# Optimization experiments

Measured on AMD Instinct MI355X. Metric: run time of the kernel, lower is better.

## Reference

```python
import jax, jax.numpy as jnp
import numpy as np

LATENT_DIM = 256
CODEBOOK_SIZE = 8192
COMMITMENT_WEIGHT = 0.25
CODEBOOK_WEIGHT = 1.0


def setup_inputs() -> dict:
    key = jax.random.key(0)
    k1, k2 = jax.random.split(key)
    latents = jax.random.normal(k1, (16, 1024, LATENT_DIM), dtype=jnp.float32)
    patch_mask = jnp.ones((16, 1024), dtype=jnp.float32)
    # nn.init.uniform_(codebook.weight, -1/K, 1/K)
    codebook = jax.random.uniform(
        k2, (CODEBOOK_SIZE, LATENT_DIM), dtype=jnp.float32,
        minval=-1.0 / CODEBOOK_SIZE, maxval=1.0 / CODEBOOK_SIZE)
    return {"latents": latents, "patch_mask": patch_mask, "codebook": codebook}


def reference(latents, patch_mask, codebook):
    B, P, D = latents.shape
    flat = latents.reshape(-1, D)  # [N, D]
    # squared euclidean distances [N, K]
    distances = (
        jnp.sum(flat * flat, axis=1, keepdims=True)
        + jnp.sum(codebook * codebook, axis=1)
        - 2.0 * flat @ codebook.T
    )
    symbol_ids = jnp.argmin(distances, axis=1)          # [N]
    quantized = codebook[symbol_ids].reshape(B, P, D)   # [B, P, D]
    symbol_ids = symbol_ids.reshape(B, P)

    st_quantized = latents + jax.lax.stop_gradient(quantized - latents)
    commitment_loss = jnp.mean((latents - jax.lax.stop_gradient(quantized)) ** 2) * COMMITMENT_WEIGHT
    codebook_loss = jnp.mean((quantized - jax.lax.stop_gradient(latents)) ** 2) * CODEBOOK_WEIGHT

    # perplexity: masked codeword usage histogram without materializing one-hot
    denom = jnp.maximum(jnp.sum(patch_mask), 1.0)
    avg_probs = jax.ops.segment_sum(
        patch_mask.reshape(-1), symbol_ids.reshape(-1),
        num_segments=CODEBOOK_SIZE) / denom
    perplexity = jnp.exp(-jnp.sum(avg_probs * jnp.log(avg_probs + 1e-8)))

    return symbol_ids, quantized, st_quantized, commitment_loss, codebook_loss, perplexity
```

## Files before the change

kernel.cpp:

```cpp
#include <hip/hip_runtime.h>
#include <math.h>

#define DD 256
#define KK 8192
#define NN 16384
#define MT 16
#define RPW 8
#define NT 512
#define NCHG 8
#define NBM (NN / MT)
#define NBLOCKS 512
#define RSTRIDE 260

#define OUT_IDS   0
#define OUT_Q     16384
#define OUT_ST    4210688
#define OUT_COMMIT 8404992
#define OUT_CBL    8404993
#define OUT_PERP   8404994

__device__ __forceinline__ float np_block128_sumsq(const float* p) {
    #pragma clang fp contract(off)
    float r0 = p[0] * p[0], r1 = p[1] * p[1], r2 = p[2] * p[2], r3 = p[3] * p[3];
    float r4 = p[4] * p[4], r5 = p[5] * p[5], r6 = p[6] * p[6], r7 = p[7] * p[7];
    for (int i = 8; i < 128; i += 8) {
        r0 = r0 + p[i + 0] * p[i + 0];
        r1 = r1 + p[i + 1] * p[i + 1];
        r2 = r2 + p[i + 2] * p[i + 2];
        r3 = r3 + p[i + 3] * p[i + 3];
        r4 = r4 + p[i + 4] * p[i + 4];
        r5 = r5 + p[i + 5] * p[i + 5];
        r6 = r6 + p[i + 6] * p[i + 6];
        r7 = r7 + p[i + 7] * p[i + 7];
    }
    return ((r0 + r1) + (r2 + r3)) + ((r4 + r5) + (r6 + r7));
}

__device__ __forceinline__ float np_pairwise256_sumsq(const float* a) {
    #pragma clang fp contract(off)
    float s0 = np_block128_sumsq(a);
    float s1 = np_block128_sumsq(a + 128);
    return s0 + s1;
}

__global__ __launch_bounds__(256) void rowsumsq(const float* __restrict__ A,
                                                float* __restrict__ out) {
    __shared__ __align__(16) float sA[64][RSTRIDE];
    const int tid = threadIdx.x;
    const int base = blockIdx.x * 64;
    #pragma unroll
    for (int i = 0; i < 16; ++i) {
        int g = i * 256 + tid;
        int row = g >> 6, d4 = g & 63;
        float4 v = reinterpret_cast<const float4*>(A)[(size_t)(base + row) * (DD / 4) + d4];
        *reinterpret_cast<float4*>(&sA[row][d4 * 4]) = v;
    }
    __syncthreads();
    if (tid < 64) out[base + tid] = np_pairwise256_sumsq(sA[tid]);
}

__global__ __launch_bounds__(256) void cb_transpose(const float* __restrict__ CB,
                                                    float4* __restrict__ CBt) {
    const int id = blockIdx.x * 256 + threadIdx.x;
    const int p   = id >> 13;
    const int col = id & (KK - 1);
    CBt[id] = *reinterpret_cast<const float4*>(CB + (size_t)col * DD + p * 4);
}

__global__ __launch_bounds__(256) void vq_main(const float* __restrict__ X,
                                               const float4* __restrict__ CBt,
                                               const float* __restrict__ c2,
                                               const float* __restrict__ x2,
                                               const float* __restrict__ mask,
                                               float* __restrict__ out,
                                               float* __restrict__ hist) {
    __shared__ float gbest[2][MT];
    __shared__ int   gidx[2][MT];

    const int tid  = threadIdx.x;
    const int lane = tid & 63;
    const int wid  = tid >> 6;
    const int widu = __builtin_amdgcn_readfirstlane(wid);
    const int g    = wid >> 1;
    const int gu   = widu >> 1;
    const int wg   = wid & 1;
    const int wgu  = widu & 1;
    const int block_row = blockIdx.x * MT;

    const float* xr = X + (size_t)(block_row + wgu * RPW) * DD;

    float x2r[RPW];
    #pragma unroll
    for (int rr = 0; rr < RPW; ++rr) x2r[rr] = x2[block_row + wg * RPW + rr];

    float best[RPW];
    int   besti[RPW];
    #pragma unroll
    for (int rr = 0; rr < RPW; ++rr) { best[rr] = 3.4e38f; besti[rr] = 0; }

    const float4* cbt_lane = CBt + lane;

    for (int ch = 0; ch < NCHG; ++ch) {
        const int chg = gu * NCHG + ch;
        float c2v[8];
        #pragma unroll
        for (int j = 0; j < 8; ++j) c2v[j] = c2[chg * NT + lane + 64 * j];

        float acc[8][8];
        #pragma unroll
        for (int rr = 0; rr < 8; ++rr)
            #pragma unroll
            for (int j = 0; j < 8; ++j) acc[rr][j] = 0.0f;

        const float4* cbase = cbt_lane + (size_t)chg * NT;

        for (int b = 0; b < 8; ++b) {
            #pragma unroll
            for (int t = 0; t < 8; ++t) {
                const int p = b * 8 + t;
                const float4* src = cbase + (size_t)p * KK;
                #pragma unroll
                for (int jh = 0; jh < 2; ++jh) {
                    float4 cc[4];
                    #pragma unroll
                    for (int j = 0; j < 4; ++j) cc[j] = src[64 * (jh * 4 + j)];
                    #pragma unroll
                    for (int rr = 0; rr < 8; ++rr) {
                        const float sx = xr[rr * DD + p * 4 + 0];
                        const float sy = xr[rr * DD + p * 4 + 1];
                        const float sz = xr[rr * DD + p * 4 + 2];
                        const float sw = xr[rr * DD + p * 4 + 3];
                        #pragma unroll
                        for (int j = 0; j < 4; ++j) {
                            float& a = acc[rr][jh * 4 + j];
                            a = fmaf(sx, cc[j].x, a);
                            a = fmaf(sy, cc[j].y, a);
                            a = fmaf(sz, cc[j].z, a);
                            a = fmaf(sw, cc[j].w, a);
                        }
                    }
                }
            }
        }

        #pragma unroll
        for (int rr = 0; rr < 8; ++rr) {
            #pragma unroll
            for (int j = 0; j < 8; ++j) {
                const int col = chg * NT + lane + 64 * j;
                float t1 = x2r[rr] + c2v[j];
                float sc = t1 - 2.0f * acc[rr][j];
                if (sc < best[rr] || (sc == best[rr] && col < besti[rr])) {
                    best[rr] = sc; besti[rr] = col;
                }
            }
        }
    }

    #pragma unroll
    for (int rr = 0; rr < RPW; ++rr) {
        float b = best[rr];
        int  bi = besti[rr];
        #pragma unroll
        for (int m = 32; m > 0; m >>= 1) {
            float b2 = __shfl_xor(b, m, 64);
            int   i2 = __shfl_xor(bi, m, 64);
            if (b2 < b || (b2 == b && i2 < bi)) { b = b2; bi = i2; }
        }
        if (lane == 0) {
            gbest[g][wg * RPW + rr] = b;
            gidx [g][wg * RPW + rr] = bi;
        }
    }
    __syncthreads();

    if (tid < MT) {
        const float b0 = gbest[0][tid], b1 = gbest[1][tid];
        const int bi = (b1 < b0) ? gidx[1][tid] : gidx[0][tid];
        out[OUT_IDS + block_row + tid] = (float)bi;
        atomicAdd(&hist[bi], mask[block_row + tid]);
    }
}

__global__ __launch_bounds__(256) void vq_gather(const float* __restrict__ X,
                                                 const float* __restrict__ CB,
                                                 float* __restrict__ out,
                                                 float* __restrict__ partial) {
    __shared__ int   row_id[32];
    __shared__ float wsum[4];
    const int tid  = threadIdx.x;
    const int lane = tid & 63;
    const int wid  = tid >> 6;
    const int block_row = blockIdx.x * 32;

    if (tid < 32) row_id[tid] = (int)out[OUT_IDS + block_row + tid];
    __syncthreads();

    float msep = 0.0f;
    float* outq  = out + OUT_Q;
    float* outst = out + OUT_ST;
    #pragma unroll
    for (int i = 0; i < 8; ++i) {
        int g2 = i * 256 + tid;
        int row = g2 >> 6;
        int d4  = g2 & 63;
        int id  = row_id[row];
        float4 q = reinterpret_cast<const float4*>(CB)[(size_t)id * (DD / 4) + d4];
        float4 x = reinterpret_cast<const float4*>(X)[(size_t)(block_row + row) * (DD / 4) + d4];
        float4 st;
        st.x = x.x + (q.x - x.x);
        st.y = x.y + (q.y - x.y);
        st.z = x.z + (q.z - x.z);
        st.w = x.w + (q.w - x.w);
        float dx = x.x - q.x; msep = fmaf(dx, dx, msep);
        dx = x.y - q.y; msep = fmaf(dx, dx, msep);
        dx = x.z - q.z; msep = fmaf(dx, dx, msep);
        dx = x.w - q.w; msep = fmaf(dx, dx, msep);
        size_t o = (size_t)(block_row + row) * (DD / 4) + d4;
        reinterpret_cast<float4*>(outq)[o]  = q;
        reinterpret_cast<float4*>(outst)[o] = st;
    }
    #pragma unroll
    for (int off = 32; off > 0; off >>= 1) msep += __shfl_down(msep, off, 64);
    if (lane == 0) wsum[wid] = msep;
    __syncthreads();
    if (tid == 0) partial[blockIdx.x] = wsum[0] + wsum[1] + wsum[2] + wsum[3];
}

__global__ __launch_bounds__(256) void vq_finalize(const float* __restrict__ partial,
                                                   const float* __restrict__ hist,
                                                   float* __restrict__ out) {
    __shared__ double red[256];
    const int tid = threadIdx.x;

    double ps = 0.0;
    for (int j = tid; j < NBLOCKS; j += 256) ps += (double)partial[j];
    red[tid] = ps;
    __syncthreads();
    for (int s = 128; s > 0; s >>= 1) {
        if (tid < s) red[tid] += red[tid + s];
        __syncthreads();
    }
    double mse_sum = red[0];
    __syncthreads();

    double hs = 0.0;
    for (int j = tid; j < KK; j += 256) hs += (double)hist[j];
    red[tid] = hs;
    __syncthreads();
    for (int s = 128; s > 0; s >>= 1) {
        if (tid < s) red[tid] += red[tid + s];
        __syncthreads();
    }
    double denom = red[0] > 1.0 ? red[0] : 1.0;
    __syncthreads();

    double ent = 0.0;
    for (int j = tid; j < KK; j += 256) {
        double p = (double)hist[j] / denom;
        ent += p * log(p + 1e-8);
    }
    red[tid] = ent;
    __syncthreads();
    for (int s = 128; s > 0; s >>= 1) {
        if (tid < s) red[tid] += red[tid + s];
        __syncthreads();
    }

    if (tid == 0) {
        double mse = mse_sum / (double)((size_t)NN * DD);
        out[OUT_COMMIT] = (float)(mse * 0.25);
        out[OUT_CBL]    = (float)mse;
        out[OUT_PERP]   = (float)exp(-red[0]);
    }
}

extern "C" void kernel_launch(void* const* d_in, const int* in_sizes, int n_in,
                              void* d_out, int out_size, void* d_ws, size_t ws_size,
                              hipStream_t stream) {
    const float* latents = (const float*)d_in[0];
    const float* mask    = (const float*)d_in[1];
    const float* cb      = (const float*)d_in[2];
    float* out = (float*)d_out;

    float* hist    = (float*)d_ws;
    float* partial = hist + KK;
    float* c2      = partial + NBLOCKS;
    float* x2      = c2 + KK;

    float4* cbt = reinterpret_cast<float4*>(out + OUT_Q);

    hipMemsetAsync(d_ws, 0, KK * sizeof(float), stream);
    rowsumsq<<<KK / 64, 256, 0, stream>>>(cb, c2);
    rowsumsq<<<NN / 64, 256, 0, stream>>>(latents, x2);
    cb_transpose<<<(64 * KK) / 256, 256, 0, stream>>>(cb, cbt);
    vq_main<<<NBM, 256, 0, stream>>>(latents, cbt, c2, x2, mask, out, hist);
    vq_gather<<<NBLOCKS, 256, 0, stream>>>(latents, cb, out, partial);
    vq_finalize<<<1, 256, 0, stream>>>(partial, hist, out);
}
```

Before: 934.1 us.

## Transpose latents and double-buffer codebook loads in distance GEMM

Adds a kernel that transposes the latents into float4-interleaved layout (stored in the st_quantized output region as scratch), so each step's 8-row x values sit contiguously. The inner loop is rewritten with two register buffers of eight float4 codebook values, prefetching the next slice while FMAs run on the current one. The aim is to hide global load latency and make the uniform x loads cheaper. The cost is an extra transpose pass over the latents and higher register pressure from sixteen float4 buffers plus the 64 accumulators.

```diff
diff --git a/kernel.cpp b/kernel.cpp
--- a/kernel.cpp
+++ b/kernel.cpp
@@ -67,7 +67,37 @@
     CBt[id] = *reinterpret_cast<const float4*>(CB + (size_t)col * DD + p * 4);
 }
 
-__global__ __launch_bounds__(256) void vq_main(const float* __restrict__ X,
+__global__ __launch_bounds__(256) void x_transpose(const float* __restrict__ X,
+                                                   float4* __restrict__ Xt) {
+    const int id = blockIdx.x * 256 + threadIdx.x;
+    const int p   = id >> 14;
+    const int row = id & (NN - 1);
+    Xt[id] = *reinterpret_cast<const float4*>(X + (size_t)row * DD + p * 4);
+}
+
+#define LOADCC(dst, ptr) do {                                                  \
+    _Pragma("unroll")                                                          \
+    for (int j_ = 0; j_ < 8; ++j_) (dst)[j_] = (ptr)[64 * j_];                 \
+} while (0)
+
+#define FMASTEP(cc, xs) do {                                                   \
+    _Pragma("unroll")                                                          \
+    for (int rr_ = 0; rr_ < 8; ++rr_) {                                        \
+        const float sx_ = (xs)[rr_ * 4 + 0];                                   \
+        const float sy_ = (xs)[rr_ * 4 + 1];                                   \
+        const float sz_ = (xs)[rr_ * 4 + 2];                                   \
+        const float sw_ = (xs)[rr_ * 4 + 3];                                   \
+        _Pragma("unroll")                                                      \
+        for (int j_ = 0; j_ < 8; ++j_) {                                       \
+            acc[rr_][j_] = fmaf(sx_, (cc)[j_].x, acc[rr_][j_]);                \
+            acc[rr_][j_] = fmaf(sy_, (cc)[j_].y, acc[rr_][j_]);                \
+            acc[rr_][j_] = fmaf(sz_, (cc)[j_].z, acc[rr_][j_]);                \
+            acc[rr_][j_] = fmaf(sw_, (cc)[j_].w, acc[rr_][j_]);                \
+        }                                                                      \
+    }                                                                          \
+} while (0)
+
+__global__ __launch_bounds__(256) void vq_main(const float4* __restrict__ Xt,
                                                const float4* __restrict__ CBt,
                                                const float* __restrict__ c2,
                                                const float* __restrict__ x2,
@@ -87,7 +117,8 @@
     const int wgu  = widu & 1;
     const int block_row = blockIdx.x * MT;
 
-    const float* xr = X + (size_t)(block_row + wgu * RPW) * DD;
+    const float* xbase = reinterpret_cast<const float*>(Xt)
+                       + (size_t)(block_row + wgu * RPW) * 4;
 
     float x2r[RPW];
     #pragma unroll
@@ -112,36 +143,24 @@
             #pragma unroll
             for (int j = 0; j < 8; ++j) acc[rr][j] = 0.0f;
 
-        const float4* cbase = cbt_lane + (size_t)chg * NT;
-
-        for (int b = 0; b < 8; ++b) {
-            #pragma unroll
-            for (int t = 0; t < 8; ++t) {
-                const int p = b * 8 + t;
-                const float4* src = cbase + (size_t)p * KK;
-                #pragma unroll
-                for (int jh = 0; jh < 2; ++jh) {
-                    float4 cc[4];
-                    #pragma unroll
-                    for (int j = 0; j < 4; ++j) cc[j] = src[64 * (jh * 4 + j)];
-                    #pragma unroll
-                    for (int rr = 0; rr < 8; ++rr) {
-                        const float sx = xr[rr * DD + p * 4 + 0];
-                        const float sy = xr[rr * DD + p * 4 + 1];
-                        const float sz = xr[rr * DD + p * 4 + 2];
-                        const float sw = xr[rr * DD + p * 4 + 3];
-                        #pragma unroll
-                        for (int j = 0; j < 4; ++j) {
-                            float& a = acc[rr][jh * 4 + j];
-                            a = fmaf(sx, cc[j].x, a);
-                            a = fmaf(sy, cc[j].y, a);
-                            a = fmaf(sz, cc[j].z, a);
-                            a = fmaf(sw, cc[j].w, a);
-                        }
-                    }
-                }
-            }
+        float4 ccA[8], ccB[8];
+        const float4* pA = cbt_lane + (size_t)chg * NT;
+        const float4* pB = pA + KK;
+        const float*  xs = xbase;
+
+        LOADCC(ccA, pA);
+        for (int pb = 0; pb < 31; ++pb) {
+            LOADCC(ccB, pB);
+            FMASTEP(ccA, xs);
+            pA += 2 * KK;
+            LOADCC(ccA, pA);
+            FMASTEP(ccB, xs + NN * 4);
+            pB += 2 * KK;
+            xs += 2 * NN * 4;
         }
+        LOADCC(ccB, pB);
+        FMASTEP(ccA, xs);
+        FMASTEP(ccB, xs + NN * 4);
 
         #pragma unroll
         for (int rr = 0; rr < 8; ++rr) {
@@ -289,12 +308,14 @@
     float* x2      = c2 + KK;
 
     float4* cbt = reinterpret_cast<float4*>(out + OUT_Q);
+    float4* xt  = reinterpret_cast<float4*>(out + OUT_ST);
 
     hipMemsetAsync(d_ws, 0, KK * sizeof(float), stream);
     rowsumsq<<<KK / 64, 256, 0, stream>>>(cb, c2);
     rowsumsq<<<NN / 64, 256, 0, stream>>>(latents, x2);
     cb_transpose<<<(64 * KK) / 256, 256, 0, stream>>>(cb, cbt);
-    vq_main<<<NBM, 256, 0, stream>>>(latents, cbt, c2, x2, mask, out, hist);
+    x_transpose<<<(64 * NN) / 256, 256, 0, stream>>>(latents, xt);
+    vq_main<<<NBM, 256, 0, stream>>>(xt, cbt, c2, x2, mask, out, hist);
     vq_gather<<<NBLOCKS, 256, 0, stream>>>(latents, cb, out, partial);
     vq_finalize<<<1, 256, 0, stream>>>(partial, hist, out);
 }
```

Measured after the change: 975.9 us. +4.5%, slower.

## Stream codebook tiles into LDS with async global_load_lds double buffering

Applied to the files above, without the earlier changes.

Changes the transposed codebook layout so that each chunk group's 64 d-slices sit contiguously. The main distance loop now prefetches each slice into a per-wave double-buffered LDS region using global_load_lds, with explicit vmcnt/lgkmcnt waits, before reading it back from LDS for the FMAs. This is meant to hide global memory latency behind compute and to stream loads sequentially. In exchange it adds 64KB of LDS per block, which can lower occupancy, and relies on hand-placed waitcnt and sched_barrier calls for correctness.

```diff
diff --git a/kernel.cpp b/kernel.cpp
--- a/kernel.cpp
+++ b/kernel.cpp
@@ -11,6 +11,7 @@
 #define NBM (NN / MT)
 #define NBLOCKS 512
 #define RSTRIDE 260
+#define NPL 512
 
 #define OUT_IDS   0
 #define OUT_Q     16384
@@ -18,6 +19,12 @@
 #define OUT_COMMIT 8404992
 #define OUT_CBL    8404993
 #define OUT_PERP   8404994
+
+__device__ __forceinline__ void gl2lds16(const float* g, float* l) {
+    __builtin_amdgcn_global_load_lds(
+        (const __attribute__((address_space(1))) float*)g,
+        (__attribute__((address_space(3))) float*)l, 16, 0, 0);
+}
 
 __device__ __forceinline__ float np_block128_sumsq(const float* p) {
     #pragma clang fp contract(off)
@@ -59,21 +66,25 @@
     if (tid < 64) out[base + tid] = np_pairwise256_sumsq(sA[tid]);
 }
 
-__global__ __launch_bounds__(256) void cb_transpose(const float* __restrict__ CB,
-                                                    float4* __restrict__ CBt) {
+__global__ __launch_bounds__(256) void cb_transpose2(const float* __restrict__ CB,
+                                                     float4* __restrict__ CBt2) {
     const int id = blockIdx.x * 256 + threadIdx.x;
-    const int p   = id >> 13;
-    const int col = id & (KK - 1);
-    CBt[id] = *reinterpret_cast<const float4*>(CB + (size_t)col * DD + p * 4);
+    const int q  = id >> 9;
+    const int cw = id & 511;
+    const int chg = q >> 6;
+    const int p   = q & 63;
+    const int col = chg * 512 + cw;
+    CBt2[id] = *reinterpret_cast<const float4*>(CB + (size_t)col * DD + p * 4);
 }
 
 __global__ __launch_bounds__(256) void vq_main(const float* __restrict__ X,
-                                               const float4* __restrict__ CBt,
+                                               const float4* __restrict__ CBt2,
                                                const float* __restrict__ c2,
                                                const float* __restrict__ x2,
                                                const float* __restrict__ mask,
                                                float* __restrict__ out,
                                                float* __restrict__ hist) {
+    __shared__ __align__(16) float sCC[4 * 4096];
     __shared__ float gbest[2][MT];
     __shared__ int   gidx[2][MT];
 
@@ -87,6 +98,11 @@
     const int wgu  = widu & 1;
     const int block_row = blockIdx.x * MT;
 
+    float* const dl0 = &sCC[widu * 4096];
+    float* const dl1 = dl0 + 2048;
+    const float* const sl0 = dl0 + lane * 4;
+    const float* const sl1 = sl0 + 2048;
+
     const float* xr = X + (size_t)(block_row + wgu * RPW) * DD;
 
     float x2r[RPW];
@@ -98,7 +114,14 @@
     #pragma unroll
     for (int rr = 0; rr < RPW; ++rr) { best[rr] = 3.4e38f; besti[rr] = 0; }
 
-    const float4* cbt_lane = CBt + lane;
+    const float4* srcq = CBt2 + (size_t)gu * NPL * 512 + lane;
+
+    #pragma unroll
+    for (int k = 0; k < 8; ++k) gl2lds16((const float*)(srcq + k * 64), dl0 + k * 256);
+    srcq += 512;
+    #pragma unroll
+    for (int k = 0; k < 8; ++k) gl2lds16((const float*)(srcq + k * 64), dl1 + k * 256);
+    srcq += 512;
 
     for (int ch = 0; ch < NCHG; ++ch) {
         const int chg = gu * NCHG + ch;
@@ -112,33 +135,42 @@
             #pragma unroll
             for (int j = 0; j < 8; ++j) acc[rr][j] = 0.0f;
 
-        const float4* cbase = cbt_lane + (size_t)chg * NT;
-
-        for (int b = 0; b < 8; ++b) {
+        #pragma unroll 2
+        for (int p = 0; p < 64; ++p) {
+            const int q = ch * 64 + p;
+
+            if (q == NPL - 1) { asm volatile("s_waitcnt vmcnt(0)" ::: "memory"); }
+            else              { asm volatile("s_waitcnt vmcnt(8)" ::: "memory"); }
+            __builtin_amdgcn_sched_barrier(0);
+
+            const float* sb = (q & 1) ? sl1 : sl0;
+            float4 cc[8];
             #pragma unroll
-            for (int t = 0; t < 8; ++t) {
-                const int p = b * 8 + t;
-                const float4* src = cbase + (size_t)p * KK;
+            for (int j = 0; j < 8; ++j)
+                cc[j] = *reinterpret_cast<const float4*>(sb + j * 256);
+            asm volatile("s_waitcnt lgkmcnt(0)" ::: "memory");
+            __builtin_amdgcn_sched_barrier(0);
+
+            if (q < NPL - 2) {
+                float* db = (q & 1) ? dl1 : dl0;
                 #pragma unroll
-                for (int jh = 0; jh < 2; ++jh) {
-                    float4 cc[4];
-                    #pragma unroll
-                    for (int j = 0; j < 4; ++j) cc[j] = src[64 * (jh * 4 + j)];
-                    #pragma unroll
-                    for (int rr = 0; rr < 8; ++rr) {
-                        const float sx = xr[rr * DD + p * 4 + 0];
-                        const float sy = xr[rr * DD + p * 4 + 1];
-                        const float sz = xr[rr * DD + p * 4 + 2];
-                        const float sw = xr[rr * DD + p * 4 + 3];
-                        #pragma unroll
-                        for (int j = 0; j < 4; ++j) {
-                            float& a = acc[rr][jh * 4 + j];
-                            a = fmaf(sx, cc[j].x, a);
-                            a = fmaf(sy, cc[j].y, a);
-                            a = fmaf(sz, cc[j].z, a);
-                            a = fmaf(sw, cc[j].w, a);
-                        }
-                    }
+                for (int k = 0; k < 8; ++k)
+                    gl2lds16((const float*)(srcq + k * 64), db + k * 256);
+                srcq += 512;
+            }
+
+            #pragma unroll
+            for (int rr = 0; rr < 8; ++rr) {
+                const float sx = xr[rr * DD + p * 4 + 0];
+                const float sy = xr[rr * DD + p * 4 + 1];
+                const float sz = xr[rr * DD + p * 4 + 2];
+                const float sw = xr[rr * DD + p * 4 + 3];
+                #pragma unroll
+                for (int j = 0; j < 8; ++j) {
+                    acc[rr][j] = fmaf(sx, cc[j].x, acc[rr][j]);
+                    acc[rr][j] = fmaf(sy, cc[j].y, acc[rr][j]);
+                    acc[rr][j] = fmaf(sz, cc[j].z, acc[rr][j]);
+                    acc[rr][j] = fmaf(sw, cc[j].w, acc[rr][j]);
                 }
             }
         }
@@ -288,13 +320,13 @@
     float* c2      = partial + NBLOCKS;
     float* x2      = c2 + KK;
 
-    float4* cbt = reinterpret_cast<float4*>(out + OUT_Q);
+    float4* cbt2 = reinterpret_cast<float4*>(out + OUT_Q);
 
     hipMemsetAsync(d_ws, 0, KK * sizeof(float), stream);
     rowsumsq<<<KK / 64, 256, 0, stream>>>(cb, c2);
     rowsumsq<<<NN / 64, 256, 0, stream>>>(latents, x2);
-    cb_transpose<<<(64 * KK) / 256, 256, 0, stream>>>(cb, cbt);
-    vq_main<<<NBM, 256, 0, stream>>>(latents, cbt, c2, x2, mask, out, hist);
+    cb_transpose2<<<(64 * KK) / 256, 256, 0, stream>>>(cb, cbt2);
+    vq_main<<<NBM, 256, 0, stream>>>(latents, cbt2, c2, x2, mask, out, hist);
     vq_gather<<<NBLOCKS, 256, 0, stream>>>(latents, cb, out, partial);
     vq_finalize<<<1, 256, 0, stream>>>(partial, hist, out);
 }
```

Result: slower. 1.088 ms (+16.5%).
